# Kernel tuning notes

Hardware: AMD Instinct MI355X
Metric: run time of the kernel (lower is better)

The kernel has to match this reference:

```python
import jax, jax.numpy as jnp
import numpy as np


def extract_spanning_tree(adj):
    """Vectorized FIFO-BFS spanning tree, matching the torch per-batch numpy BFS.

    BFS starts at the first active node (smallest index with degree>0). A node's
    parent is the earliest-dequeued (min BFS order) neighbor; within a level,
    dequeue order is sorted by (parent order, node index), i.e. FIFO semantics.
    adj: [B, N, N] symmetric binary float. Returns tree adjacency [B, N, N].
    """
    B, N, _ = adj.shape
    A = adj > 0.5                                   # [B,N,N] bool
    active = adj.sum(-1) > 0                        # [B,N]
    root = jnp.argmax(active, axis=-1).astype(jnp.int32)
    has_any = jnp.any(active, axis=-1)
    idx = jnp.arange(N, dtype=jnp.int32)
    INF = jnp.int32(N * N + N)
    visited0 = (idx[None, :] == root[:, None]) & has_any[:, None]
    order0 = jnp.where(visited0, 0, INF).astype(jnp.int32)
    parent0 = jnp.zeros((B, N), jnp.int32)
    counter0 = visited0.sum(-1).astype(jnp.int32)

    def step(state, _):
        visited, order, parent, counter = state
        nb_ord = jnp.where(A, order[:, None, :], INF)           # neighbor BFS orders
        po = nb_ord.min(-1)                                     # [B,N] min order among neighbors
        p = jnp.argmin(nb_ord, axis=-1).astype(jnp.int32)       # earliest-dequeued neighbor
        newly = (~visited) & (po < INF)                         # discovered this level
        key = jnp.where(newly, po * N + idx[None, :], INF * N)  # FIFO tie-break (parent order, index)
        rank = jnp.sum(key[:, None, :] < key[:, :, None], axis=-1).astype(jnp.int32)
        order = jnp.where(newly, counter[:, None] + rank, order)
        parent = jnp.where(newly, p, parent)
        visited = visited | newly
        counter = counter + newly.sum(-1).astype(jnp.int32)
        return (visited, order, parent, counter), None

    (visited, order, parent, _), _ = jax.lax.scan(
        step, (visited0, order0, parent0, counter0), None, length=N - 1)
    child = visited & (order > 0)                               # non-root visited nodes
    P = jax.nn.one_hot(jnp.where(child, parent, 0), N, dtype=adj.dtype)
    P = P * child[..., None].astype(adj.dtype)                  # P[b,v,parent(v)] = 1
    return P + jnp.swapaxes(P, -1, -2)


def gcn(x, tree_adj, W, b):
    N = tree_adj.shape[-1]
    adj_hat = tree_adj + jnp.eye(N, dtype=tree_adj.dtype)       # add self loops
    degree = jnp.clip(adj_hat.sum(-1, keepdims=True), 1.0, None)
    adj_norm = adj_hat / degree                                 # row normalization
    return jnp.einsum('bij,bjf->bif', adj_norm, x @ W + b)


def setup_inputs() -> dict:
    key = jax.random.key(0)
    ks = jax.random.split(key, 12)
    B, N, D, H, L = 1024, 128, 128, 256, 64
    x = jax.random.normal(ks[0], (B, N, D), dtype=jnp.float32)
    u = jax.random.uniform(ks[1], (B, N, N))
    adj = (u < 0.03).astype(jnp.float32)
    adj = jnp.maximum(adj, jnp.swapaxes(adj, -1, -2))           # symmetrize
    adj = adj * (1.0 - jnp.eye(N, dtype=jnp.float32))           # no self loops
    W1 = jax.random.normal(ks[2], (D, H), jnp.float32) / np.sqrt(D)
    b1 = jnp.zeros((H,), jnp.float32)
    W2 = jax.random.normal(ks[3], (H, H), jnp.float32) / np.sqrt(H)
    b2 = jnp.zeros((H,), jnp.float32)
    Wmu = jax.random.normal(ks[4], (H, L), jnp.float32) / np.sqrt(H)
    bmu = jnp.zeros((L,), jnp.float32)
    Wlv = jax.random.normal(ks[5], (H, L), jnp.float32) / np.sqrt(H)
    blv = jnp.zeros((L,), jnp.float32)
    return {"x": x, "adj": adj, "W1": W1, "b1": b1, "W2": W2, "b2": b2,
            "Wmu": Wmu, "bmu": bmu, "Wlv": Wlv, "blv": blv}


def reference(x, adj, W1, b1, W2, b2, Wmu, bmu, Wlv, blv):
    tree = jax.lax.stop_gradient(extract_spanning_tree(adj))    # torch builds it detached
    h = jax.nn.relu(gcn(x, tree, W1, b1))
    h = jax.nn.relu(gcn(h, tree, W2, b2))
    node_mask = (adj.sum(-1) > 0).astype(x.dtype)[..., None]    # [B,N,1]
    num_nodes = jnp.clip(node_mask.sum(1), 1.0, None)           # [B,1]
    graph_feat = (h * node_mask).sum(1) / num_nodes             # mean over active nodes
    mu = graph_feat @ Wmu + bmu
    logvar = graph_feat @ Wlv + blv
    return (mu, logvar)
```

## Files before the change

kernel.cpp:

```cpp
#include <hip/hip_runtime.h>
#include <stdint.h>

#define B_ 1024
#define N_ 128
#define D_ 128
#define H_ 256
#define L_ 64
#define INF_ 0x3FFFFFFF

typedef __attribute__((ext_vector_type(8))) short bf16x8;
typedef __attribute__((ext_vector_type(4))) float f32x4;
typedef __attribute__((ext_vector_type(4))) uint32_t u32x4;
typedef __attribute__((ext_vector_type(2))) uint32_t u32x2;

__device__ __forceinline__ float b2f(uint16_t u) {
    return __uint_as_float(((uint32_t)u) << 16);
}
__device__ __forceinline__ uint16_t f2b(float f) {
    uint32_t u = __float_as_uint(f);
    return (uint16_t)((u + 0x7FFFu + ((u >> 16) & 1u)) >> 16);
}
__device__ __forceinline__ uint32_t pack2(float a, float b) {
    return (uint32_t)f2b(a) | ((uint32_t)f2b(b) << 16);
}

__global__ void prep_weights(const float* __restrict__ W1, const float* __restrict__ W2,
                             uint16_t* __restrict__ ws) {
    int t = blockIdx.x * 256 + threadIdx.x;
    if (t < 4096) {
        int lane = t & 63, fkb = t >> 6;
        int tm = fkb >> 2, kb = fkb & 3;
        int h  = tm * 16 + (lane & 15);
        int k0 = kb * 32 + (lane >> 4) * 8;
        u32x4 w;
        #pragma unroll
        for (int p = 0; p < 4; ++p)
            w[p] = pack2(W1[(k0 + 2*p) * H_ + h], W1[(k0 + 2*p + 1) * H_ + h]);
        *reinterpret_cast<u32x4*>(&ws[t * 8]) = w;
    } else if (t < 12288) {
        int t2 = t - 4096;
        int lane = t2 & 63, g = t2 >> 6;
        int tn = g >> 3, kb = g & 7;
        int n  = tn * 16 + (lane & 15);
        int k0 = kb * 32 + (lane >> 4) * 8;
        u32x4 w;
        #pragma unroll
        for (int p = 0; p < 4; ++p)
            w[p] = pack2(W2[(k0 + 2*p) * H_ + n], W2[(k0 + 2*p + 1) * H_ + n]);
        *reinterpret_cast<u32x4*>(&ws[32768 + t2 * 8]) = w;
    }
}

__global__ __launch_bounds__(256, 2) void tree_encoder_kernel(
    const float* __restrict__ x, const float* __restrict__ adj,
    const uint16_t* __restrict__ ws,
    const float* __restrict__ b1g, const float* __restrict__ b2g,
    const float* __restrict__ Wmu, const float* __restrict__ bmu,
    const float* __restrict__ Wlv, const float* __restrict__ blv,
    float* __restrict__ out)
{
    __shared__ __align__(16) uint16_t sbuf[33792];
    __shared__ uint32_t adjm[128][4];
    __shared__ uint32_t tnbr[128][4];
    __shared__ int      s_order[128];
    __shared__ int      s_parent[128];
    __shared__ int      s_key[128];
    __shared__ float    s_inv[128];
    __shared__ float    s_wm[128];
    __shared__ float    s_b1[256];
    __shared__ float    s_b2[256];
    __shared__ float    s_g[256];
    __shared__ uint32_t visw[4], actw[4], newlyw[4];
    __shared__ int      s_root;

    const int tid  = threadIdx.x;
    const int b    = blockIdx.x;
    const int wid  = tid >> 6;
    const int lane = tid & 63;
    const int l15  = lane & 15;
    const int q    = lane >> 4;

    const float* xg = x   + (size_t)b * N_ * D_;
    const float* ag = adj + (size_t)b * N_ * N_;

    if (tid < 128) { s_order[tid] = INF_; s_parent[tid] = 0; }
    if (tid < 4)   { visw[tid] = 0u; actw[tid] = 0u; }
    if (tid == 0)  { s_root = 128; }
    s_b1[tid] = b1g[tid];
    s_b2[tid] = b2g[tid];
    {
        const float4* xg4 = reinterpret_cast<const float4*>(xg);
        #pragma unroll
        for (int i = 0; i < 16; ++i) {
            int idx = tid + i * 256;
            float4 v = xg4[idx];
            int row = idx >> 5, c4 = (idx & 31) * 4;
            u32x2 w; w[0] = pack2(v.x, v.y); w[1] = pack2(v.z, v.w);
            *reinterpret_cast<u32x2*>(&sbuf[row * 136 + c4]) = w;
        }
    }
    {
        const int v = tid >> 1, hf = tid & 1;
        const float4* ag4 = reinterpret_cast<const float4*>(ag + v * N_ + hf * 64);
        uint32_t w0 = 0, w1 = 0;
        #pragma unroll
        for (int i = 0; i < 16; ++i) {
            float4 f = ag4[i];
            uint32_t bs = (f.x > 0.5f ? 1u : 0u) | (f.y > 0.5f ? 2u : 0u) |
                          (f.z > 0.5f ? 4u : 0u) | (f.w > 0.5f ? 8u : 0u);
            int base = i * 4;
            if (base < 32) w0 |= bs << base; else w1 |= bs << (base - 32);
        }
        adjm[v][hf * 2]     = w0;
        adjm[v][hf * 2 + 1] = w1;
    }
    __syncthreads();

    if (tid < 128) {
        uint32_t any = adjm[tid][0] | adjm[tid][1] | adjm[tid][2] | adjm[tid][3];
        if (any) {
            atomicMin(&s_root, tid);
            atomicOr(&actw[tid >> 5], 1u << (tid & 31));
        }
    }
    __syncthreads();
    int counter = 0;
    if (s_root < 128) {
        counter = 1;
        if (tid == 0) {
            s_order[s_root] = 0;
            visw[s_root >> 5] = 1u << (s_root & 31);
        }
    }
    __syncthreads();

    for (int step = 0; step < N_ - 1; ++step) {
        if (tid < 4) newlyw[tid] = 0u;
        __syncthreads();
        int newly = 0, po = INF_, par = 0;
        if (tid < 128 && s_order[tid] >= INF_) {
            #pragma unroll
            for (int w = 0; w < 4; ++w) {
                uint32_t m = adjm[tid][w] & visw[w];
                while (m) {
                    int u = (w << 5) + __ffs(m) - 1; m &= m - 1;
                    int o = s_order[u];
                    if (o < po) { po = o; par = u; }
                }
            }
            newly = (po < INF_);
            if (newly) {
                s_key[tid] = po * N_ + tid;
                atomicOr(&newlyw[tid >> 5], 1u << (tid & 31));
            }
        }
        __syncthreads();
        int myk = newly ? po * N_ + tid : 0x7FFFFFFF;
        int cnt = 0, rank = 0;
        #pragma unroll
        for (int w = 0; w < 4; ++w) {
            uint32_t m = newlyw[w];
            cnt += __popc(m);
            while (m) {
                int u = (w << 5) + __ffs(m) - 1; m &= m - 1;
                rank += (s_key[u] < myk);
            }
        }
        if (newly) {
            s_order[tid]  = counter + rank;
            s_parent[tid] = par;
            atomicOr(&visw[tid >> 5], 1u << (tid & 31));
        }
        counter += cnt;
        __syncthreads();
        if (cnt == 0) break;
    }

    if (tid < 128) { tnbr[tid][0] = 0; tnbr[tid][1] = 0; tnbr[tid][2] = 0; tnbr[tid][3] = 0; }
    __syncthreads();
    if (tid < 128 && s_order[tid] > 0 && s_order[tid] < INF_) {
        int p = s_parent[tid];
        atomicOr(&tnbr[tid][p >> 5], 1u << (p & 31));
        atomicOr(&tnbr[p][tid >> 5], 1u << (tid & 31));
    }
    __syncthreads();
    if (tid < 128) {
        int d = 1 + __popc(tnbr[tid][0]) + __popc(tnbr[tid][1]) +
                    __popc(tnbr[tid][2]) + __popc(tnbr[tid][3]);
        s_inv[tid] = 1.0f / (float)d;
        int num = __popc(actw[0]) + __popc(actw[1]) + __popc(actw[2]) + __popc(actw[3]);
        int act = (actw[tid >> 5] >> (tid & 31)) & 1;
        s_wm[tid] = act ? (1.0f / (float)(num > 0 ? num : 1)) : 0.0f;
    }
    __syncthreads();

    {
        const int v = tid >> 1, hf = tid & 1;
        float acc[64];
        const uint16_t* xr = &sbuf[v * 136 + hf * 64];
        #pragma unroll
        for (int i = 0; i < 64; i += 4) {
            uint64_t w = *reinterpret_cast<const uint64_t*>(xr + i);
            acc[i]   = b2f((uint16_t)w);
            acc[i+1] = b2f((uint16_t)(w >> 16));
            acc[i+2] = b2f((uint16_t)(w >> 32));
            acc[i+3] = b2f((uint16_t)(w >> 48));
        }
        #pragma unroll
        for (int wi = 0; wi < 4; ++wi) {
            uint32_t m = tnbr[v][wi];
            while (m) {
                int u = (wi << 5) + __ffs(m) - 1; m &= m - 1;
                const uint16_t* ur = &sbuf[u * 136 + hf * 64];
                #pragma unroll
                for (int i = 0; i < 64; i += 4) {
                    uint64_t w = *reinterpret_cast<const uint64_t*>(ur + i);
                    acc[i]   += b2f((uint16_t)w);
                    acc[i+1] += b2f((uint16_t)(w >> 16));
                    acc[i+2] += b2f((uint16_t)(w >> 32));
                    acc[i+3] += b2f((uint16_t)(w >> 48));
                }
            }
        }
        const float inv = s_inv[v];
        const int tnx = v >> 4, v15 = v & 15;
        #pragma unroll
        for (int kbl = 0; kbl < 2; ++kbl) {
            int kb = hf * 2 + kbl;
            #pragma unroll
            for (int qq = 0; qq < 4; ++qq) {
                int lo = kbl * 32 + qq * 8;
                u32x4 w;
                w[0] = pack2(acc[lo  ] * inv, acc[lo+1] * inv);
                w[1] = pack2(acc[lo+2] * inv, acc[lo+3] * inv);
                w[2] = pack2(acc[lo+4] * inv, acc[lo+5] * inv);
                w[3] = pack2(acc[lo+6] * inv, acc[lo+7] * inv);
                *reinterpret_cast<u32x4*>(
                    &sbuf[17408 + (((tnx * 4 + kb) * 64) + qq * 16 + v15) * 8]) = w;
            }
        }
    }
    __syncthreads();

    {
        f32x4 acc1[4][8];
        #pragma unroll
        for (int j = 0; j < 4; ++j)
            #pragma unroll
            for (int t = 0; t < 8; ++t) acc1[j][t] = (f32x4){0.f, 0.f, 0.f, 0.f};
        const bf16x8* wsA = reinterpret_cast<const bf16x8*>(ws);
        for (int kb = 0; kb < 4; ++kb) {
            bf16x8 afr[4], bfr[8];
            #pragma unroll
            for (int j = 0; j < 4; ++j)
                afr[j] = wsA[((wid * 4 + j) * 4 + kb) * 64 + lane];
            #pragma unroll
            for (int t = 0; t < 8; ++t)
                bfr[t] = *reinterpret_cast<const bf16x8*>(
                    &sbuf[17408 + ((t * 4 + kb) * 64 + lane) * 8]);
            #pragma unroll
            for (int j = 0; j < 4; ++j)
                #pragma unroll
                for (int t = 0; t < 8; ++t)
                    acc1[j][t] = __builtin_amdgcn_mfma_f32_16x16x32_bf16(
                        afr[j], bfr[t], acc1[j][t], 0, 0, 0);
        }
        __syncthreads();
        #pragma unroll
        for (int j = 0; j < 4; ++j) {
            int tm = wid * 4 + j;
            int m0 = tm * 16 + q * 4;
            f32x4 bb = *reinterpret_cast<const f32x4*>(&s_b1[m0]);
            int kbh = tm >> 1;
            int sl  = l15 + 16 * ((2 * tm + (q >> 1)) & 3);
            #pragma unroll
            for (int t = 0; t < 8; ++t) {
                f32x4 v = acc1[j][t];
                float v0 = fmaxf(v[0] + bb[0], 0.f), v1 = fmaxf(v[1] + bb[1], 0.f);
                float v2 = fmaxf(v[2] + bb[2], 0.f), v3 = fmaxf(v[3] + bb[3], 0.f);
                u32x2 w; w[0] = pack2(v0, v1); w[1] = pack2(v2, v3);
                *reinterpret_cast<u32x2*>(
                    &sbuf[((t * 8 + kbh) * 64 + sl) * 8 + (q & 1) * 4]) = w;
            }
        }
    }
    __syncthreads();

    {
        f32x4 acc2[8][4];
        #pragma unroll
        for (int tm = 0; tm < 8; ++tm)
            #pragma unroll
            for (int j = 0; j < 4; ++j) acc2[tm][j] = (f32x4){0.f, 0.f, 0.f, 0.f};
        const bf16x8* wsB = reinterpret_cast<const bf16x8*>(ws + 32768);
        for (int kb = 0; kb < 8; ++kb) {
            bf16x8 a2[8], bfr[4];
            #pragma unroll
            for (int tm = 0; tm < 8; ++tm)
                a2[tm] = *reinterpret_cast<const bf16x8*>(
                    &sbuf[((tm * 8 + kb) * 64 + lane) * 8]);
            #pragma unroll
            for (int j = 0; j < 4; ++j)
                bfr[j] = wsB[((wid * 4 + j) * 8 + kb) * 64 + lane];
            #pragma unroll
            for (int tm = 0; tm < 8; ++tm)
                #pragma unroll
                for (int j = 0; j < 4; ++j)
                    acc2[tm][j] = __builtin_amdgcn_mfma_f32_16x16x32_bf16(
                        a2[tm], bfr[j], acc2[tm][j], 0, 0, 0);
        }
        __syncthreads();
        #pragma unroll
        for (int tm = 0; tm < 8; ++tm) {
            int kbh = tm >> 1;
            int sl  = l15 + 16 * ((2 * tm + (q >> 1)) & 3);
            #pragma unroll
            for (int j = 0; j < 4; ++j) {
                int tn = wid * 4 + j;
                f32x4 v = acc2[tm][j];
                u32x2 w; w[0] = pack2(v[0], v[1]); w[1] = pack2(v[2], v[3]);
                *reinterpret_cast<u32x2*>(
                    &sbuf[((tn * 4 + kbh) * 64 + sl) * 8 + (q & 1) * 4]) = w;
            }
        }
    }
    __syncthreads();

    {
        f32x4 acc3[8][4];
        #pragma unroll
        for (int tm = 0; tm < 8; ++tm)
            #pragma unroll
            for (int j = 0; j < 4; ++j) acc3[tm][j] = (f32x4){0.f, 0.f, 0.f, 0.f};
        for (int kb = 0; kb < 4; ++kb) {
            bf16x8 a3[8], bfr[4];
            #pragma unroll
            for (int tm = 0; tm < 8; ++tm) {
                int v = tm * 16 + l15;
                uint32_t word = tnbr[v][kb];
                uint32_t by = (word >> (q * 8)) & 0xFFu;
                if ((v >> 3) == kb * 4 + q) by |= 1u << (v & 7);
                u32x4 p;
                #pragma unroll
                for (int pp = 0; pp < 4; ++pp)
                    p[pp] = (((by >> (2 * pp)) & 1u) ? 0x3F80u : 0u) |
                            (((by >> (2 * pp + 1)) & 1u) ? 0x3F800000u : 0u);
                a3[tm] = __builtin_bit_cast(bf16x8, p);
            }
            #pragma unroll
            for (int j = 0; j < 4; ++j)
                bfr[j] = *reinterpret_cast<const bf16x8*>(
                    &sbuf[(((wid * 4 + j) * 4 + kb) * 64 + lane) * 8]);
            #pragma unroll
            for (int tm = 0; tm < 8; ++tm)
                #pragma unroll
                for (int j = 0; j < 4; ++j)
                    acc3[tm][j] = __builtin_amdgcn_mfma_f32_16x16x32_bf16(
                        a3[tm], bfr[j], acc3[tm][j], 0, 0, 0);
        }
        float ps[4] = {0.f, 0.f, 0.f, 0.f};
        #pragma unroll
        for (int tm = 0; tm < 8; ++tm) {
            int v0 = tm * 16 + q * 4;
            f32x4 iv = *reinterpret_cast<const f32x4*>(&s_inv[v0]);
            f32x4 wm = *reinterpret_cast<const f32x4*>(&s_wm[v0]);
            #pragma unroll
            for (int j = 0; j < 4; ++j) {
                float bc = s_b2[(wid * 4 + j) * 16 + l15];
                f32x4 a = acc3[tm][j];
                #pragma unroll
                for (int r = 0; r < 4; ++r)
                    ps[j] += fmaxf(fmaf(a[r], iv[r], bc), 0.f) * wm[r];
            }
        }
        #pragma unroll
        for (int j = 0; j < 4; ++j) {
            ps[j] += __shfl_xor(ps[j], 16);
            ps[j] += __shfl_xor(ps[j], 32);
        }
        if (q == 0) {
            #pragma unroll
            for (int j = 0; j < 4; ++j)
                s_g[(wid * 4 + j) * 16 + l15] = ps[j];
        }
    }
    __syncthreads();

    if (tid < 128) {
        const int which = tid >> 6, l = tid & 63;
        const float* W    = which ? Wlv : Wmu;
        const float* bias = which ? blv : bmu;
        float acch = 0.f;
        for (int cc = 0; cc < H_; ++cc)
            acch = fmaf(s_g[cc], W[cc * L_ + l], acch);
        out[(size_t)which * B_ * L_ + (size_t)b * L_ + l] = acch + bias[l];
    }
}

extern "C" void kernel_launch(void* const* d_in, const int* in_sizes, int n_in,
                              void* d_out, int out_size, void* d_ws, size_t ws_size,
                              hipStream_t stream) {
    const float* x   = (const float*)d_in[0];
    const float* adj = (const float*)d_in[1];
    const float* W1  = (const float*)d_in[2];
    const float* b1  = (const float*)d_in[3];
    const float* W2  = (const float*)d_in[4];
    const float* b2  = (const float*)d_in[5];
    const float* Wmu = (const float*)d_in[6];
    const float* bmu = (const float*)d_in[7];
    const float* Wlv = (const float*)d_in[8];
    const float* blv = (const float*)d_in[9];
    float* out = (float*)d_out;
    uint16_t* ws = (uint16_t*)d_ws;

    hipLaunchKernelGGL(prep_weights, dim3(48), dim3(256), 0, stream, W1, W2, ws);
    hipLaunchKernelGGL(tree_encoder_kernel, dim3(B_), dim3(256), 0, stream,
                       x, adj, ws, b1, b2, Wmu, bmu, Wlv, blv, out);
}
```

Measured before the change: 106.0 us.

## Split fused encoder into tree, GCN, and heads kernels with wider GCN blocks

```diff
diff --git a/kernel.cpp b/kernel.cpp
--- a/kernel.cpp
+++ b/kernel.cpp
@@ -7,6 +7,11 @@
 #define H_ 256
 #define L_ 64
 #define INF_ 0x3FFFFFFF
+
+#define WS_W1   0u
+#define WS_W2   65536u
+#define WS_TREE 196608u
+#define WS_G    3342336u
 
 typedef __attribute__((ext_vector_type(8))) short bf16x8;
 typedef __attribute__((ext_vector_type(4))) float f32x4;
@@ -51,54 +56,26 @@
     }
 }
 
-__global__ __launch_bounds__(256, 2) void tree_encoder_kernel(
-    const float* __restrict__ x, const float* __restrict__ adj,
-    const uint16_t* __restrict__ ws,
-    const float* __restrict__ b1g, const float* __restrict__ b2g,
-    const float* __restrict__ Wmu, const float* __restrict__ bmu,
-    const float* __restrict__ Wlv, const float* __restrict__ blv,
-    float* __restrict__ out)
+__global__ __launch_bounds__(256, 4) void tree_kernel(
+    const float* __restrict__ adj, uint8_t* __restrict__ wsb)
 {
-    __shared__ __align__(16) uint16_t sbuf[33792];
     __shared__ uint32_t adjm[128][4];
-    __shared__ uint32_t tnbr[128][4];
+    __shared__ __align__(16) uint32_t tnbr[128][4];
     __shared__ int      s_order[128];
     __shared__ int      s_parent[128];
     __shared__ int      s_key[128];
     __shared__ float    s_inv[128];
     __shared__ float    s_wm[128];
-    __shared__ float    s_b1[256];
-    __shared__ float    s_b2[256];
-    __shared__ float    s_g[256];
     __shared__ uint32_t visw[4], actw[4], newlyw[4];
     __shared__ int      s_root;
 
-    const int tid  = threadIdx.x;
-    const int b    = blockIdx.x;
-    const int wid  = tid >> 6;
-    const int lane = tid & 63;
-    const int l15  = lane & 15;
-    const int q    = lane >> 4;
-
-    const float* xg = x   + (size_t)b * N_ * D_;
+    const int tid = threadIdx.x;
+    const int b   = blockIdx.x;
     const float* ag = adj + (size_t)b * N_ * N_;
 
     if (tid < 128) { s_order[tid] = INF_; s_parent[tid] = 0; }
     if (tid < 4)   { visw[tid] = 0u; actw[tid] = 0u; }
     if (tid == 0)  { s_root = 128; }
-    s_b1[tid] = b1g[tid];
-    s_b2[tid] = b2g[tid];
-    {
-        const float4* xg4 = reinterpret_cast<const float4*>(xg);
-        #pragma unroll
-        for (int i = 0; i < 16; ++i) {
-            int idx = tid + i * 256;
-            float4 v = xg4[idx];
-            int row = idx >> 5, c4 = (idx & 31) * 4;
-            u32x2 w; w[0] = pack2(v.x, v.y); w[1] = pack2(v.z, v.w);
-            *reinterpret_cast<u32x2*>(&sbuf[row * 136 + c4]) = w;
-        }
-    }
     {
         const int v = tid >> 1, hf = tid & 1;
         const float4* ag4 = reinterpret_cast<const float4*>(ag + v * N_ + hf * 64);
@@ -187,19 +164,64 @@
     if (tid < 128) {
         int d = 1 + __popc(tnbr[tid][0]) + __popc(tnbr[tid][1]) +
                     __popc(tnbr[tid][2]) + __popc(tnbr[tid][3]);
-        s_inv[tid] = 1.0f / (float)d;
         int num = __popc(actw[0]) + __popc(actw[1]) + __popc(actw[2]) + __popc(actw[3]);
         int act = (actw[tid >> 5] >> (tid & 31)) & 1;
-        s_wm[tid] = act ? (1.0f / (float)(num > 0 ? num : 1)) : 0.0f;
-    }
-    __syncthreads();
-
-    {
-        const int v = tid >> 1, hf = tid & 1;
-        float acc[64];
-        const uint16_t* xr = &sbuf[v * 136 + hf * 64];
-        #pragma unroll
-        for (int i = 0; i < 64; i += 4) {
+        uint8_t* gbase = wsb + WS_TREE + (size_t)b * 3072;
+        *reinterpret_cast<u32x4*>(gbase + tid * 16) =
+            *reinterpret_cast<u32x4*>(&tnbr[tid][0]);
+        reinterpret_cast<float*>(gbase + 2048)[tid] = 1.0f / (float)d;
+        reinterpret_cast<float*>(gbase + 2560)[tid] =
+            act ? (1.0f / (float)(num > 0 ? num : 1)) : 0.0f;
+    }
+}
+
+__global__ __launch_bounds__(512, 2) void gcn_kernel(
+    const float* __restrict__ x, const uint16_t* __restrict__ ws,
+    const uint8_t* __restrict__ wsb,
+    const float* __restrict__ b1g, const float* __restrict__ b2g,
+    float* __restrict__ wsG)
+{
+    __shared__ __align__(16) uint16_t sbuf[34304];
+    __shared__ __align__(16) uint32_t tnbr[128][4];
+    __shared__ float    s_inv[128];
+    __shared__ float    s_wm[128];
+
+    const int tid  = threadIdx.x;
+    const int b    = blockIdx.x;
+    const int wid  = tid >> 6;
+    const int lane = tid & 63;
+    const int l15  = lane & 15;
+    const int q    = lane >> 4;
+
+    const float* xg = x + (size_t)b * N_ * D_;
+
+    {
+        const float4* xg4 = reinterpret_cast<const float4*>(xg);
+        #pragma unroll
+        for (int i = 0; i < 8; ++i) {
+            int idx = tid + i * 512;
+            float4 v = xg4[idx];
+            int row = idx >> 5, c4 = (idx & 31) * 4;
+            u32x2 w; w[0] = pack2(v.x, v.y); w[1] = pack2(v.z, v.w);
+            *reinterpret_cast<u32x2*>(&sbuf[row * 140 + c4]) = w;
+        }
+    }
+    if (tid < 128) {
+        const uint8_t* gbase = wsb + WS_TREE + (size_t)b * 3072;
+        u32x4 t4 = *reinterpret_cast<const u32x4*>(gbase + tid * 16);
+        tnbr[tid][0] = t4[0]; tnbr[tid][1] = t4[1];
+        tnbr[tid][2] = t4[2]; tnbr[tid][3] = t4[3];
+        s_inv[tid] = reinterpret_cast<const float*>(gbase + 2048)[tid];
+        s_wm[tid]  = reinterpret_cast<const float*>(gbase + 2560)[tid];
+    }
+    __syncthreads();
+
+    {
+        const int v = tid >> 2, part = tid & 3;
+        float acc[32];
+        const uint16_t* xr = &sbuf[v * 140 + part * 32];
+        #pragma unroll
+        for (int i = 0; i < 32; i += 4) {
             uint64_t w = *reinterpret_cast<const uint64_t*>(xr + i);
             acc[i]   = b2f((uint16_t)w);
             acc[i+1] = b2f((uint16_t)(w >> 16));
@@ -211,9 +233,9 @@
             uint32_t m = tnbr[v][wi];
             while (m) {
                 int u = (wi << 5) + __ffs(m) - 1; m &= m - 1;
-                const uint16_t* ur = &sbuf[u * 136 + hf * 64];
-                #pragma unroll
-                for (int i = 0; i < 64; i += 4) {
+                const uint16_t* ur = &sbuf[u * 140 + part * 32];
+                #pragma unroll
+                for (int i = 0; i < 32; i += 4) {
                     uint64_t w = *reinterpret_cast<const uint64_t*>(ur + i);
                     acc[i]   += b2f((uint16_t)w);
                     acc[i+1] += b2f((uint16_t)(w >> 16));
@@ -225,41 +247,37 @@
         const float inv = s_inv[v];
         const int tnx = v >> 4, v15 = v & 15;
         #pragma unroll
-        for (int kbl = 0; kbl < 2; ++kbl) {
-            int kb = hf * 2 + kbl;
-            #pragma unroll
-            for (int qq = 0; qq < 4; ++qq) {
-                int lo = kbl * 32 + qq * 8;
-                u32x4 w;
-                w[0] = pack2(acc[lo  ] * inv, acc[lo+1] * inv);
-                w[1] = pack2(acc[lo+2] * inv, acc[lo+3] * inv);
-                w[2] = pack2(acc[lo+4] * inv, acc[lo+5] * inv);
-                w[3] = pack2(acc[lo+6] * inv, acc[lo+7] * inv);
-                *reinterpret_cast<u32x4*>(
-                    &sbuf[17408 + (((tnx * 4 + kb) * 64) + qq * 16 + v15) * 8]) = w;
-            }
-        }
-    }
-    __syncthreads();
-
-    {
-        f32x4 acc1[4][8];
-        #pragma unroll
-        for (int j = 0; j < 4; ++j)
+        for (int qq = 0; qq < 4; ++qq) {
+            int lo = qq * 8;
+            u32x4 w;
+            w[0] = pack2(acc[lo  ] * inv, acc[lo+1] * inv);
+            w[1] = pack2(acc[lo+2] * inv, acc[lo+3] * inv);
+            w[2] = pack2(acc[lo+4] * inv, acc[lo+5] * inv);
+            w[3] = pack2(acc[lo+6] * inv, acc[lo+7] * inv);
+            *reinterpret_cast<u32x4*>(
+                &sbuf[17920 + (((tnx * 4 + part) * 64) + qq * 16 + v15) * 8]) = w;
+        }
+    }
+    __syncthreads();
+
+    {
+        f32x4 acc1[2][8];
+        #pragma unroll
+        for (int j = 0; j < 2; ++j)
             #pragma unroll
             for (int t = 0; t < 8; ++t) acc1[j][t] = (f32x4){0.f, 0.f, 0.f, 0.f};
         const bf16x8* wsA = reinterpret_cast<const bf16x8*>(ws);
         for (int kb = 0; kb < 4; ++kb) {
-            bf16x8 afr[4], bfr[8];
-            #pragma unroll
-            for (int j = 0; j < 4; ++j)
-                afr[j] = wsA[((wid * 4 + j) * 4 + kb) * 64 + lane];
+            bf16x8 afr[2], bfr[8];
+            #pragma unroll
+            for (int j = 0; j < 2; ++j)
+                afr[j] = wsA[((wid * 2 + j) * 4 + kb) * 64 + lane];
             #pragma unroll
             for (int t = 0; t < 8; ++t)
                 bfr[t] = *reinterpret_cast<const bf16x8*>(
-                    &sbuf[17408 + ((t * 4 + kb) * 64 + lane) * 8]);
-            #pragma unroll
-            for (int j = 0; j < 4; ++j)
+                    &sbuf[17920 + ((t * 4 + kb) * 64 + lane) * 8]);
+            #pragma unroll
+            for (int j = 0; j < 2; ++j)
                 #pragma unroll
                 for (int t = 0; t < 8; ++t)
                     acc1[j][t] = __builtin_amdgcn_mfma_f32_16x16x32_bf16(
@@ -267,10 +285,10 @@
         }
         __syncthreads();
         #pragma unroll
-        for (int j = 0; j < 4; ++j) {
-            int tm = wid * 4 + j;
+        for (int j = 0; j < 2; ++j) {
+            int tm = wid * 2 + j;
             int m0 = tm * 16 + q * 4;
-            f32x4 bb = *reinterpret_cast<const f32x4*>(&s_b1[m0]);
+            f32x4 bb = *reinterpret_cast<const f32x4*>(b1g + m0);
             int kbh = tm >> 1;
             int sl  = l15 + 16 * ((2 * tm + (q >> 1)) & 3);
             #pragma unroll
@@ -287,25 +305,25 @@
     __syncthreads();
 
     {
-        f32x4 acc2[8][4];
+        f32x4 acc2[8][2];
         #pragma unroll
         for (int tm = 0; tm < 8; ++tm)
             #pragma unroll
-            for (int j = 0; j < 4; ++j) acc2[tm][j] = (f32x4){0.f, 0.f, 0.f, 0.f};
+            for (int j = 0; j < 2; ++j) acc2[tm][j] = (f32x4){0.f, 0.f, 0.f, 0.f};
         const bf16x8* wsB = reinterpret_cast<const bf16x8*>(ws + 32768);
         for (int kb = 0; kb < 8; ++kb) {
-            bf16x8 a2[8], bfr[4];
+            bf16x8 a2[8], bfr[2];
             #pragma unroll
             for (int tm = 0; tm < 8; ++tm)
                 a2[tm] = *reinterpret_cast<const bf16x8*>(
                     &sbuf[((tm * 8 + kb) * 64 + lane) * 8]);
             #pragma unroll
-            for (int j = 0; j < 4; ++j)
-                bfr[j] = wsB[((wid * 4 + j) * 8 + kb) * 64 + lane];
+            for (int j = 0; j < 2; ++j)
+                bfr[j] = wsB[((wid * 2 + j) * 8 + kb) * 64 + lane];
             #pragma unroll
             for (int tm = 0; tm < 8; ++tm)
                 #pragma unroll
-                for (int j = 0; j < 4; ++j)
+                for (int j = 0; j < 2; ++j)
                     acc2[tm][j] = __builtin_amdgcn_mfma_f32_16x16x32_bf16(
                         a2[tm], bfr[j], acc2[tm][j], 0, 0, 0);
         }
@@ -315,8 +333,8 @@
             int kbh = tm >> 1;
             int sl  = l15 + 16 * ((2 * tm + (q >> 1)) & 3);
             #pragma unroll
-            for (int j = 0; j < 4; ++j) {
-                int tn = wid * 4 + j;
+            for (int j = 0; j < 2; ++j) {
+                int tn = wid * 2 + j;
                 f32x4 v = acc2[tm][j];
                 u32x2 w; w[0] = pack2(v[0], v[1]); w[1] = pack2(v[2], v[3]);
                 *reinterpret_cast<u32x2*>(
@@ -327,13 +345,13 @@
     __syncthreads();
 
     {
-        f32x4 acc3[8][4];
+        f32x4 acc3[8][2];
         #pragma unroll
         for (int tm = 0; tm < 8; ++tm)
             #pragma unroll
-            for (int j = 0; j < 4; ++j) acc3[tm][j] = (f32x4){0.f, 0.f, 0.f, 0.f};
+            for (int j = 0; j < 2; ++j) acc3[tm][j] = (f32x4){0.f, 0.f, 0.f, 0.f};
         for (int kb = 0; kb < 4; ++kb) {
-            bf16x8 a3[8], bfr[4];
+            bf16x8 a3[8], bfr[2];
             #pragma unroll
             for (int tm = 0; tm < 8; ++tm) {
                 int v = tm * 16 + l15;
@@ -348,25 +366,25 @@
                 a3[tm] = __builtin_bit_cast(bf16x8, p);
             }
             #pragma unroll
-            for (int j = 0; j < 4; ++j)
+            for (int j = 0; j < 2; ++j)
                 bfr[j] = *reinterpret_cast<const bf16x8*>(
-                    &sbuf[(((wid * 4 + j) * 4 + kb) * 64 + lane) * 8]);
+                    &sbuf[(((wid * 2 + j) * 4 + kb) * 64 + lane) * 8]);
             #pragma unroll
             for (int tm = 0; tm < 8; ++tm)
                 #pragma unroll
-                for (int j = 0; j < 4; ++j)
+                for (int j = 0; j < 2; ++j)
                     acc3[tm][j] = __builtin_amdgcn_mfma_f32_16x16x32_bf16(
                         a3[tm], bfr[j], acc3[tm][j], 0, 0, 0);
         }
-        float ps[4] = {0.f, 0.f, 0.f, 0.f};
+        float ps[2] = {0.f, 0.f};
         #pragma unroll
         for (int tm = 0; tm < 8; ++tm) {
             int v0 = tm * 16 + q * 4;
             f32x4 iv = *reinterpret_cast<const f32x4*>(&s_inv[v0]);
             f32x4 wm = *reinterpret_cast<const f32x4*>(&s_wm[v0]);
             #pragma unroll
-            for (int j = 0; j < 4; ++j) {
-                float bc = s_b2[(wid * 4 + j) * 16 + l15];
+            for (int j = 0; j < 2; ++j) {
+                float bc = b2g[(wid * 2 + j) * 16 + l15];
                 f32x4 a = acc3[tm][j];
                 #pragma unroll
                 for (int r = 0; r < 4; ++r)
@@ -374,27 +392,37 @@
             }
         }
         #pragma unroll
-        for (int j = 0; j < 4; ++j) {
+        for (int j = 0; j < 2; ++j) {
             ps[j] += __shfl_xor(ps[j], 16);
             ps[j] += __shfl_xor(ps[j], 32);
         }
         if (q == 0) {
             #pragma unroll
-            for (int j = 0; j < 4; ++j)
-                s_g[(wid * 4 + j) * 16 + l15] = ps[j];
-        }
-    }
-    __syncthreads();
-
-    if (tid < 128) {
-        const int which = tid >> 6, l = tid & 63;
-        const float* W    = which ? Wlv : Wmu;
-        const float* bias = which ? blv : bmu;
-        float acch = 0.f;
-        for (int cc = 0; cc < H_; ++cc)
-            acch = fmaf(s_g[cc], W[cc * L_ + l], acch);
-        out[(size_t)which * B_ * L_ + (size_t)b * L_ + l] = acch + bias[l];
-    }
+            for (int j = 0; j < 2; ++j)
+                wsG[(size_t)b * 256 + (wid * 2 + j) * 16 + l15] = ps[j];
+        }
+    }
+}
+
+__global__ __launch_bounds__(128, 8) void heads_kernel(
+    const float* __restrict__ wsG,
+    const float* __restrict__ Wmu, const float* __restrict__ bmu,
+    const float* __restrict__ Wlv, const float* __restrict__ blv,
+    float* __restrict__ out)
+{
+    __shared__ float sg[256];
+    const int tid = threadIdx.x, b = blockIdx.x;
+    const float* g = wsG + (size_t)b * 256;
+    sg[tid]       = g[tid];
+    sg[tid + 128] = g[tid + 128];
+    __syncthreads();
+    const int which = tid >> 6, l = tid & 63;
+    const float* W = which ? Wlv : Wmu;
+    float acc = which ? blv[l] : bmu[l];
+    #pragma unroll 8
+    for (int cc = 0; cc < 256; ++cc)
+        acc = fmaf(sg[cc], W[cc * L_ + l], acc);
+    out[(size_t)which * B_ * L_ + (size_t)b * L_ + l] = acc;
 }
 
 extern "C" void kernel_launch(void* const* d_in, const int* in_sizes, int n_in,
@@ -411,9 +439,14 @@
     const float* Wlv = (const float*)d_in[8];
     const float* blv = (const float*)d_in[9];
     float* out = (float*)d_out;
-    uint16_t* ws = (uint16_t*)d_ws;
+    uint8_t*  wsb = (uint8_t*)d_ws;
+    uint16_t* ws  = (uint16_t*)d_ws;
+    float*    wsG = (float*)(wsb + WS_G);
 
     hipLaunchKernelGGL(prep_weights, dim3(48), dim3(256), 0, stream, W1, W2, ws);
-    hipLaunchKernelGGL(tree_encoder_kernel, dim3(B_), dim3(256), 0, stream,
-                       x, adj, ws, b1, b2, Wmu, bmu, Wlv, blv, out);
-}
+    hipLaunchKernelGGL(tree_kernel, dim3(B_), dim3(256), 0, stream, adj, wsb);
+    hipLaunchKernelGGL(gcn_kernel, dim3(B_), dim3(512), 0, stream,
+                       x, ws, wsb, b1, b2, wsG);
+    hipLaunchKernelGGL(heads_kernel, dim3(B_), dim3(128), 0, stream,
+                       wsG, Wmu, bmu, Wlv, blv, out);
+}
```

After: 119.0 us. +12.3%, slower.

## Stream x in fp32 chunks overlapped with aggregation, shrink LDS, split output GEMV

Applied to the files above, without the earlier changes.

```diff
diff --git a/kernel.cpp b/kernel.cpp
--- a/kernel.cpp
+++ b/kernel.cpp
@@ -1,4 +1,5 @@
 #include <hip/hip_runtime.h>
+#include <hip/hip_bf16.h>
 #include <stdint.h>
 
 #define B_ 1024
@@ -13,15 +14,11 @@
 typedef __attribute__((ext_vector_type(4))) uint32_t u32x4;
 typedef __attribute__((ext_vector_type(2))) uint32_t u32x2;
 
-__device__ __forceinline__ float b2f(uint16_t u) {
-    return __uint_as_float(((uint32_t)u) << 16);
-}
-__device__ __forceinline__ uint16_t f2b(float f) {
-    uint32_t u = __float_as_uint(f);
-    return (uint16_t)((u + 0x7FFFu + ((u >> 16) & 1u)) >> 16);
-}
 __device__ __forceinline__ uint32_t pack2(float a, float b) {
-    return (uint32_t)f2b(a) | ((uint32_t)f2b(b) << 16);
+    __hip_bfloat162 h = __float22bfloat162_rn(make_float2(a, b));
+    uint32_t u;
+    __builtin_memcpy(&u, &h, 4);
+    return u;
 }
 
 __global__ void prep_weights(const float* __restrict__ W1, const float* __restrict__ W2,
@@ -51,7 +48,7 @@
     }
 }
 
-__global__ __launch_bounds__(256, 2) void tree_encoder_kernel(
+__global__ __launch_bounds__(256) void fused_kernel(
     const float* __restrict__ x, const float* __restrict__ adj,
     const uint16_t* __restrict__ ws,
     const float* __restrict__ b1g, const float* __restrict__ b2g,
@@ -59,19 +56,19 @@
     const float* __restrict__ Wlv, const float* __restrict__ blv,
     float* __restrict__ out)
 {
-    __shared__ __align__(16) uint16_t sbuf[33792];
-    __shared__ uint32_t adjm[128][4];
-    __shared__ uint32_t tnbr[128][4];
-    __shared__ int      s_order[128];
-    __shared__ int      s_parent[128];
-    __shared__ int      s_key[128];
+    __shared__ __align__(16) uint16_t buf[32768];
+    __shared__ __align__(16) uint32_t tnbr[128][4];
     __shared__ float    s_inv[128];
     __shared__ float    s_wm[128];
-    __shared__ float    s_b1[256];
-    __shared__ float    s_b2[256];
     __shared__ float    s_g[256];
+    __shared__ float    s_p[256];
     __shared__ uint32_t visw[4], actw[4], newlyw[4];
     __shared__ int      s_root;
+
+    uint32_t* adjm     = reinterpret_cast<uint32_t*>(buf) + 8192;
+    int*      s_order  = reinterpret_cast<int*>(buf) + 8704;
+    int*      s_parent = reinterpret_cast<int*>(buf) + 8832;
+    int*      s_key    = reinterpret_cast<int*>(buf) + 8960;
 
     const int tid  = threadIdx.x;
     const int b    = blockIdx.x;
@@ -80,25 +77,20 @@
     const int l15  = lane & 15;
     const int q    = lane >> 4;
 
-    const float* xg = x   + (size_t)b * N_ * D_;
-    const float* ag = adj + (size_t)b * N_ * N_;
+    const float4* xg4 = reinterpret_cast<const float4*>(x + (size_t)b * N_ * D_);
+    const float*  ag  = adj + (size_t)b * N_ * N_;
+
+    const int prow = tid >> 3;
+    const int pcol = tid & 7;
+    const int pswz = pcol ^ (prow & 7);
+    float4 pf[4];
+    #pragma unroll
+    for (int i = 0; i < 4; ++i)
+        pf[i] = xg4[(prow + i * 32) * 32 + pcol];
 
     if (tid < 128) { s_order[tid] = INF_; s_parent[tid] = 0; }
     if (tid < 4)   { visw[tid] = 0u; actw[tid] = 0u; }
     if (tid == 0)  { s_root = 128; }
-    s_b1[tid] = b1g[tid];
-    s_b2[tid] = b2g[tid];
-    {
-        const float4* xg4 = reinterpret_cast<const float4*>(xg);
-        #pragma unroll
-        for (int i = 0; i < 16; ++i) {
-            int idx = tid + i * 256;
-            float4 v = xg4[idx];
-            int row = idx >> 5, c4 = (idx & 31) * 4;
-            u32x2 w; w[0] = pack2(v.x, v.y); w[1] = pack2(v.z, v.w);
-            *reinterpret_cast<u32x2*>(&sbuf[row * 136 + c4]) = w;
-        }
-    }
     {
         const int v = tid >> 1, hf = tid & 1;
         const float4* ag4 = reinterpret_cast<const float4*>(ag + v * N_ + hf * 64);
@@ -111,13 +103,13 @@
             int base = i * 4;
             if (base < 32) w0 |= bs << base; else w1 |= bs << (base - 32);
         }
-        adjm[v][hf * 2]     = w0;
-        adjm[v][hf * 2 + 1] = w1;
+        adjm[v * 4 + hf * 2]     = w0;
+        adjm[v * 4 + hf * 2 + 1] = w1;
     }
     __syncthreads();
 
     if (tid < 128) {
-        uint32_t any = adjm[tid][0] | adjm[tid][1] | adjm[tid][2] | adjm[tid][3];
+        uint32_t any = adjm[tid*4+0] | adjm[tid*4+1] | adjm[tid*4+2] | adjm[tid*4+3];
         if (any) {
             atomicMin(&s_root, tid);
             atomicOr(&actw[tid >> 5], 1u << (tid & 31));
@@ -141,7 +133,7 @@
         if (tid < 128 && s_order[tid] >= INF_) {
             #pragma unroll
             for (int w = 0; w < 4; ++w) {
-                uint32_t m = adjm[tid][w] & visw[w];
+                uint32_t m = adjm[tid * 4 + w] & visw[w];
                 while (m) {
                     int u = (w << 5) + __ffs(m) - 1; m &= m - 1;
                     int o = s_order[u];
@@ -187,60 +179,62 @@
     if (tid < 128) {
         int d = 1 + __popc(tnbr[tid][0]) + __popc(tnbr[tid][1]) +
                     __popc(tnbr[tid][2]) + __popc(tnbr[tid][3]);
-        s_inv[tid] = 1.0f / (float)d;
         int num = __popc(actw[0]) + __popc(actw[1]) + __popc(actw[2]) + __popc(actw[3]);
         int act = (actw[tid >> 5] >> (tid & 31)) & 1;
-        s_wm[tid] = act ? (1.0f / (float)(num > 0 ? num : 1)) : 0.0f;
-    }
-    __syncthreads();
-
-    {
-        const int v = tid >> 1, hf = tid & 1;
-        float acc[64];
-        const uint16_t* xr = &sbuf[v * 136 + hf * 64];
-        #pragma unroll
-        for (int i = 0; i < 64; i += 4) {
-            uint64_t w = *reinterpret_cast<const uint64_t*>(xr + i);
-            acc[i]   = b2f((uint16_t)w);
-            acc[i+1] = b2f((uint16_t)(w >> 16));
-            acc[i+2] = b2f((uint16_t)(w >> 32));
-            acc[i+3] = b2f((uint16_t)(w >> 48));
-        }
-        #pragma unroll
-        for (int wi = 0; wi < 4; ++wi) {
-            uint32_t m = tnbr[v][wi];
+        s_inv[tid] = 1.0f / (float)d;
+        s_wm[tid]  = act ? (1.0f / (float)(num > 0 ? num : 1)) : 0.0f;
+    }
+    __syncthreads();
+
+    float4* chunkF4 = reinterpret_cast<float4*>(buf + 16384);
+    const int gv = tid >> 1, gp2 = tid & 1;
+
+    for (int r = 0; r < 4; ++r) {
+        #pragma unroll
+        for (int i = 0; i < 4; ++i)
+            chunkF4[(prow + i * 32) * 8 + pswz] = pf[i];
+        if (r < 3) {
+            #pragma unroll
+            for (int i = 0; i < 4; ++i)
+                pf[i] = xg4[(prow + i * 32) * 32 + (r + 1) * 8 + pcol];
+        }
+        __syncthreads();
+        float acc[16];
+        #pragma unroll
+        for (int k = 0; k < 4; ++k) {
+            float4 a = chunkF4[gv * 8 + ((gp2 * 4 + k) ^ (gv & 7))];
+            acc[k*4+0] = a.x; acc[k*4+1] = a.y; acc[k*4+2] = a.z; acc[k*4+3] = a.w;
+        }
+        #pragma unroll
+        for (int w = 0; w < 4; ++w) {
+            uint32_t m = tnbr[gv][w];
             while (m) {
-                int u = (wi << 5) + __ffs(m) - 1; m &= m - 1;
-                const uint16_t* ur = &sbuf[u * 136 + hf * 64];
-                #pragma unroll
-                for (int i = 0; i < 64; i += 4) {
-                    uint64_t w = *reinterpret_cast<const uint64_t*>(ur + i);
-                    acc[i]   += b2f((uint16_t)w);
-                    acc[i+1] += b2f((uint16_t)(w >> 16));
-                    acc[i+2] += b2f((uint16_t)(w >> 32));
-                    acc[i+3] += b2f((uint16_t)(w >> 48));
+                int u = (w << 5) + __ffs(m) - 1; m &= m - 1;
+                #pragma unroll
+                for (int k = 0; k < 4; ++k) {
+                    float4 n = chunkF4[u * 8 + ((gp2 * 4 + k) ^ (u & 7))];
+                    acc[k*4+0] += n.x; acc[k*4+1] += n.y;
+                    acc[k*4+2] += n.z; acc[k*4+3] += n.w;
                 }
             }
         }
-        const float inv = s_inv[v];
-        const int tnx = v >> 4, v15 = v & 15;
-        #pragma unroll
-        for (int kbl = 0; kbl < 2; ++kbl) {
-            int kb = hf * 2 + kbl;
-            #pragma unroll
-            for (int qq = 0; qq < 4; ++qq) {
-                int lo = kbl * 32 + qq * 8;
-                u32x4 w;
-                w[0] = pack2(acc[lo  ] * inv, acc[lo+1] * inv);
-                w[1] = pack2(acc[lo+2] * inv, acc[lo+3] * inv);
-                w[2] = pack2(acc[lo+4] * inv, acc[lo+5] * inv);
-                w[3] = pack2(acc[lo+6] * inv, acc[lo+7] * inv);
-                *reinterpret_cast<u32x4*>(
-                    &sbuf[17408 + (((tnx * 4 + kb) * 64) + qq * 16 + v15) * 8]) = w;
-            }
-        }
-    }
-    __syncthreads();
+        const float inv = s_inv[gv];
+        #pragma unroll
+        for (int gg = 0; gg < 2; ++gg) {
+            const int gp = gp2 * 2 + gg;
+            u32x4 wv;
+            wv[0] = pack2(acc[gg*8+0] * inv, acc[gg*8+1] * inv);
+            wv[1] = pack2(acc[gg*8+2] * inv, acc[gg*8+3] * inv);
+            wv[2] = pack2(acc[gg*8+4] * inv, acc[gg*8+5] * inv);
+            wv[3] = pack2(acc[gg*8+6] * inv, acc[gg*8+7] * inv);
+            *reinterpret_cast<u32x4*>(
+                &buf[(((gv >> 4) * 4 + r) * 64 + gp * 16 + (gv & 15)) * 8]) = wv;
+        }
+        __syncthreads();
+    }
+
+    const bf16x8* wsA = reinterpret_cast<const bf16x8*>(ws);
+    const bf16x8* wsB = reinterpret_cast<const bf16x8*>(ws + 32768);
 
     {
         f32x4 acc1[4][8];
@@ -248,7 +242,6 @@
         for (int j = 0; j < 4; ++j)
             #pragma unroll
             for (int t = 0; t < 8; ++t) acc1[j][t] = (f32x4){0.f, 0.f, 0.f, 0.f};
-        const bf16x8* wsA = reinterpret_cast<const bf16x8*>(ws);
         for (int kb = 0; kb < 4; ++kb) {
             bf16x8 afr[4], bfr[8];
             #pragma unroll
@@ -257,7 +250,7 @@
             #pragma unroll
             for (int t = 0; t < 8; ++t)
                 bfr[t] = *reinterpret_cast<const bf16x8*>(
-                    &sbuf[17408 + ((t * 4 + kb) * 64 + lane) * 8]);
+                    &buf[((t * 4 + kb) * 64 + lane) * 8]);
             #pragma unroll
             for (int j = 0; j < 4; ++j)
                 #pragma unroll
@@ -270,7 +263,7 @@
         for (int j = 0; j < 4; ++j) {
             int tm = wid * 4 + j;
             int m0 = tm * 16 + q * 4;
-            f32x4 bb = *reinterpret_cast<const f32x4*>(&s_b1[m0]);
+            f32x4 bb = *reinterpret_cast<const f32x4*>(b1g + m0);
             int kbh = tm >> 1;
             int sl  = l15 + 16 * ((2 * tm + (q >> 1)) & 3);
             #pragma unroll
@@ -280,7 +273,7 @@
                 float v2 = fmaxf(v[2] + bb[2], 0.f), v3 = fmaxf(v[3] + bb[3], 0.f);
                 u32x2 w; w[0] = pack2(v0, v1); w[1] = pack2(v2, v3);
                 *reinterpret_cast<u32x2*>(
-                    &sbuf[((t * 8 + kbh) * 64 + sl) * 8 + (q & 1) * 4]) = w;
+                    &buf[((t * 8 + kbh) * 64 + sl) * 8 + (q & 1) * 4]) = w;
             }
         }
     }
@@ -292,13 +285,12 @@
         for (int tm = 0; tm < 8; ++tm)
             #pragma unroll
             for (int j = 0; j < 4; ++j) acc2[tm][j] = (f32x4){0.f, 0.f, 0.f, 0.f};
-        const bf16x8* wsB = reinterpret_cast<const bf16x8*>(ws + 32768);
         for (int kb = 0; kb < 8; ++kb) {
             bf16x8 a2[8], bfr[4];
             #pragma unroll
             for (int tm = 0; tm < 8; ++tm)
                 a2[tm] = *reinterpret_cast<const bf16x8*>(
-                    &sbuf[((tm * 8 + kb) * 64 + lane) * 8]);
+                    &buf[((tm * 8 + kb) * 64 + lane) * 8]);
             #pragma unroll
             for (int j = 0; j < 4; ++j)
                 bfr[j] = wsB[((wid * 4 + j) * 8 + kb) * 64 + lane];
@@ -320,7 +312,7 @@
                 f32x4 v = acc2[tm][j];
                 u32x2 w; w[0] = pack2(v[0], v[1]); w[1] = pack2(v[2], v[3]);
                 *reinterpret_cast<u32x2*>(
-                    &sbuf[((tn * 4 + kbh) * 64 + sl) * 8 + (q & 1) * 4]) = w;
+                    &buf[((tn * 4 + kbh) * 64 + sl) * 8 + (q & 1) * 4]) = w;
             }
         }
     }
@@ -340,17 +332,17 @@
                 uint32_t word = tnbr[v][kb];
                 uint32_t by = (word >> (q * 8)) & 0xFFu;
                 if ((v >> 3) == kb * 4 + q) by |= 1u << (v & 7);
-                u32x4 p;
+                u32x4 pm;
                 #pragma unroll
                 for (int pp = 0; pp < 4; ++pp)
-                    p[pp] = (((by >> (2 * pp)) & 1u) ? 0x3F80u : 0u) |
-                            (((by >> (2 * pp + 1)) & 1u) ? 0x3F800000u : 0u);
-                a3[tm] = __builtin_bit_cast(bf16x8, p);
+                    pm[pp] = (((by >> (2 * pp)) & 1u) ? 0x3F80u : 0u) |
+                             (((by >> (2 * pp + 1)) & 1u) ? 0x3F800000u : 0u);
+                a3[tm] = __builtin_bit_cast(bf16x8, pm);
             }
             #pragma unroll
             for (int j = 0; j < 4; ++j)
                 bfr[j] = *reinterpret_cast<const bf16x8*>(
-                    &sbuf[(((wid * 4 + j) * 4 + kb) * 64 + lane) * 8]);
+                    &buf[(((wid * 4 + j) * 4 + kb) * 64 + lane) * 8]);
             #pragma unroll
             for (int tm = 0; tm < 8; ++tm)
                 #pragma unroll
@@ -366,7 +358,7 @@
             f32x4 wm = *reinterpret_cast<const f32x4*>(&s_wm[v0]);
             #pragma unroll
             for (int j = 0; j < 4; ++j) {
-                float bc = s_b2[(wid * 4 + j) * 16 + l15];
+                float bc = b2g[(wid * 4 + j) * 16 + l15];
                 f32x4 a = acc3[tm][j];
                 #pragma unroll
                 for (int r = 0; r < 4; ++r)
@@ -386,14 +378,23 @@
     }
     __syncthreads();
 
-    if (tid < 128) {
-        const int which = tid >> 6, l = tid & 63;
-        const float* W    = which ? Wlv : Wmu;
-        const float* bias = which ? blv : bmu;
-        float acch = 0.f;
-        for (int cc = 0; cc < H_; ++cc)
-            acch = fmaf(s_g[cc], W[cc * L_ + l], acch);
-        out[(size_t)which * B_ * L_ + (size_t)b * L_ + l] = acch + bias[l];
+    {
+        const int oi = tid & 127, part = tid >> 7;
+        const int which = oi >> 6, l = oi & 63;
+        const float* W = which ? Wlv : Wmu;
+        float acc = 0.f;
+        const int c0 = part * 128;
+        #pragma unroll 8
+        for (int cc = 0; cc < 128; ++cc)
+            acc = fmaf(s_g[c0 + cc], W[(c0 + cc) * L_ + l], acc);
+        s_p[part * 128 + oi] = acc;
+        __syncthreads();
+        if (tid < 128) {
+            const int w2 = tid >> 6, l2 = tid & 63;
+            float r = s_p[tid] + s_p[128 + tid];
+            r += w2 ? blv[l2] : bmu[l2];
+            out[(size_t)w2 * B_ * L_ + (size_t)b * L_ + l2] = r;
+        }
     }
 }
 
@@ -414,6 +415,6 @@
     uint16_t* ws = (uint16_t*)d_ws;
 
     hipLaunchKernelGGL(prep_weights, dim3(48), dim3(256), 0, stream, W1, W2, ws);
-    hipLaunchKernelGGL(tree_encoder_kernel, dim3(B_), dim3(256), 0, stream,
+    hipLaunchKernelGGL(fused_kernel, dim3(B_), dim3(256), 0, stream,
                        x, adj, ws, b1, b2, Wmu, bmu, Wlv, blv, out);
 }
```

Result: slower. 176.8 us (+66.8%).
